# Optimization experiments

Measured on AMD Instinct MI355X. Metric: run time of the kernel, lower is better.

Reference implementation:

```python
import jax, jax.numpy as jnp
import numpy as np
import math

IN_CH = 32
OUT_CH = 32
NODE_NUM = 24
BATCH = 32768
# skeleton edges: self-loops + chain (parent -> child), matching init_kwargs
_SRC = list(range(24)) + list(range(23))
_DST = list(range(24)) + list(range(1, 24))


def _build_mask():
    # block mask: block (dst, src) of size [OUT_CH, IN_CH] set to 1 per edge
    m = np.zeros((OUT_CH * NODE_NUM, IN_CH * NODE_NUM), dtype=np.float32)
    for s, d in zip(_SRC, _DST):
        m[OUT_CH * d:OUT_CH * (d + 1), IN_CH * s:IN_CH * (s + 1)] = 1.0
    return jnp.asarray(m)


def setup_inputs() -> dict:
    key = jax.random.key(0)
    kx, kw, kb = jax.random.split(key, 3)
    mask = _build_mask()
    dim = IN_CH * NODE_NUM
    # kaiming-uniform-like per-block init approximated by scaled normal; only
    # values inside mask blocks matter (forward multiplies by mask anyway)
    weight = jax.random.normal(kw, (OUT_CH * NODE_NUM, dim), dtype=jnp.float32) * (1.0 / math.sqrt(IN_CH))
    bound = 1.0 / math.sqrt(dim)
    bias = jax.random.uniform(kb, (OUT_CH * NODE_NUM,), dtype=jnp.float32, minval=-bound, maxval=bound)
    x = jax.random.normal(kx, (BATCH, dim), dtype=jnp.float32)
    return {"x": x, "weight": weight, "bias": bias, "mask": mask}


def reference(x, weight, bias, mask):
    # F.linear(x, weight * mask, bias) == x @ (weight*mask)^T + bias
    w = weight * mask
    return jnp.einsum("bi,oi->bo", x, w) + bias
```

## Files before the change

kernel.cpp:

```cpp
#include <hip/hip_runtime.h>
#include <hip/hip_bf16.h>


typedef __bf16 bf16x8 __attribute__((ext_vector_type(8)));
typedef float  f32x4  __attribute__((ext_vector_type(4)));

#define DIM 768
#define STRIDE 772
#define NFRAG (24 * 2 * 2)

__device__ __forceinline__ bf16x8 cvt8(const float* __restrict__ p) {
    float4 lo = *(const float4*)p;
    float4 hi = *(const float4*)(p + 4);
    bf16x8 r;
    r[0] = (__bf16)lo.x; r[1] = (__bf16)lo.y; r[2] = (__bf16)lo.z; r[3] = (__bf16)lo.w;
    r[4] = (__bf16)hi.x; r[5] = (__bf16)hi.y; r[6] = (__bf16)hi.z; r[7] = (__bf16)hi.w;
    return r;
}

__device__ __forceinline__ bf16x8 cvt8r(float4 lo, float4 hi) {
    bf16x8 r;
    r[0] = (__bf16)lo.x; r[1] = (__bf16)lo.y; r[2] = (__bf16)lo.z; r[3] = (__bf16)lo.w;
    r[4] = (__bf16)hi.x; r[5] = (__bf16)hi.y; r[6] = (__bf16)hi.z; r[7] = (__bf16)hi.w;
    return r;
}

__global__ void prepack_w_kernel(const float* __restrict__ w, bf16x8* __restrict__ ws)
{
    const int fid = blockIdx.x * 256 + threadIdx.x;
    const int lane = fid & 63;
    const int ni   = (fid >> 6) & 1;
    const int kt   = (fid >> 7) & 1;
    const int d    = fid >> 8;
    const int quad = lane >> 4, l16 = lane & 15;

    bf16x8 v;
    if (d == 0 && kt == 0) {
#pragma unroll
        for (int j = 0; j < 8; ++j) v[j] = (__bf16)0.f;
    } else {
        const float* src = w + (long)(32 * d + 16 * ni + l16) * DIM
                             + (32 * d - 32 + 32 * kt + 8 * quad);
        v = cvt8(src);
    }
    ws[fid] = v;
}

__global__ __launch_bounds__(512, 4)
void skeleton_linear_kernel(const float* __restrict__ x,
                            const float* __restrict__ bias,
                            const bf16x8* __restrict__ wfrag,
                            float* __restrict__ out)
{
    __shared__ float lds[16 * STRIDE];

    const int tid  = threadIdx.x;
    const int lane = tid & 63;
    const int wave = tid >> 6;
    const int quad = lane >> 4;
    const int l16  = lane & 15;
    const long row = (long)blockIdx.x * 16 + l16;

    const float* xr = x + row * DIM + 8 * quad;
    float4 lo[4], hi[4];
#pragma unroll
    for (int s = 0; s < 4; ++s) {
        int kb = 32 * (3 * wave - 1 + s);
        if (kb < 0) kb = 0;
        lo[s] = *(const float4*)(xr + kb);
        hi[s] = *(const float4*)(xr + kb + 4);
    }

    bf16x8 xf[4];
#pragma unroll
    for (int s = 0; s < 4; ++s) xf[s] = cvt8r(lo[s], hi[s]);

#pragma unroll
    for (int i = 0; i < 3; ++i) {
        const int d = 3 * wave + i;
        f32x4 acc0 = *(const f32x4*)(bias + 32 * d + 4 * quad);
        f32x4 acc1 = *(const f32x4*)(bias + 32 * d + 16 + 4 * quad);
#pragma unroll
        for (int kt = 0; kt < 2; ++kt) {
            const int fb = (d * 2 + kt) * 2 * 64 + lane;
            acc0 = __builtin_amdgcn_mfma_f32_16x16x32_bf16(wfrag[fb],      xf[i + kt], acc0, 0, 0, 0);
            acc1 = __builtin_amdgcn_mfma_f32_16x16x32_bf16(wfrag[fb + 64], xf[i + kt], acc1, 0, 0, 0);
        }
        *(f32x4*)&lds[l16 * STRIDE + 32 * d + 4 * quad]      = acc0;
        *(f32x4*)&lds[l16 * STRIDE + 32 * d + 16 + 4 * quad] = acc1;
    }
    __syncthreads();

    {
        float* go = out + (long)blockIdx.x * 16 * DIM;
#pragma unroll
        for (int i = 0; i < 6; ++i) {
            int f = tid + 512 * i;
            int r = f / 192, c4 = f % 192;
            float4 v = *(const float4*)&lds[r * STRIDE + 4 * c4];
            *(float4*)(go + (long)r * DIM + 4 * c4) = v;
        }
    }
}

extern "C" void kernel_launch(void* const* d_in, const int* in_sizes, int n_in,
                              void* d_out, int out_size, void* d_ws, size_t ws_size,
                              hipStream_t stream) {
    const float* x    = (const float*)d_in[0];
    const float* w    = (const float*)d_in[1];
    const float* bias = (const float*)d_in[2];
    float* out = (float*)d_out;

    bf16x8* wpack = (bf16x8*)d_ws;

    prepack_w_kernel<<<NFRAG * 64 / 256, 256, 0, stream>>>(w, wpack);

    const int BATCH = 32768;
    dim3 grid(BATCH / 16);
    skeleton_linear_kernel<<<grid, 512, 0, stream>>>(x, bias, wpack, out);
}
```

Measured before the change: 190.1 us.

## Process two row strips per block with prefetch of next strip's inputs

Each block now handles two 16-row strips in sequence, loading the second strip's x values from global memory while the first strip is converted, multiplied and stored. This halves the grid size and aims to overlap global load latency with MFMA compute and output stores. It also raises the launch-bounds occupancy hint from 4 to 6 blocks, which puts pressure on registers. The cost is an extra barrier between strips and more live registers per thread.

```diff
diff --git a/kernel.cpp b/kernel.cpp
--- a/kernel.cpp
+++ b/kernel.cpp
@@ -8,6 +8,7 @@
 #define DIM 768
 #define STRIDE 772
 #define NFRAG (24 * 2 * 2)
+#define SPB 2
 
 __device__ __forceinline__ bf16x8 cvt8(const float* __restrict__ p) {
     float4 lo = *(const float4*)p;
@@ -46,7 +47,7 @@
     ws[fid] = v;
 }
 
-__global__ __launch_bounds__(512, 4)
+__global__ __launch_bounds__(512, 6)
 void skeleton_linear_kernel(const float* __restrict__ x,
                             const float* __restrict__ bias,
                             const bf16x8* __restrict__ wfrag,
@@ -59,47 +60,66 @@
     const int wave = tid >> 6;
     const int quad = lane >> 4;
     const int l16  = lane & 15;
-    const long row = (long)blockIdx.x * 16 + l16;
+    const long row0 = (long)blockIdx.x * (16 * SPB) + l16;
 
-    const float* xr = x + row * DIM + 8 * quad;
+    int kb[4];
+#pragma unroll
+    for (int s = 0; s < 4; ++s) {
+        int k = 32 * (3 * wave - 1 + s);
+        kb[s] = k < 0 ? 0 : k;
+    }
+
+    const float* xr = x + row0 * DIM + 8 * quad;
+
     float4 lo[4], hi[4];
 #pragma unroll
     for (int s = 0; s < 4; ++s) {
-        int kb = 32 * (3 * wave - 1 + s);
-        if (kb < 0) kb = 0;
-        lo[s] = *(const float4*)(xr + kb);
-        hi[s] = *(const float4*)(xr + kb + 4);
+        lo[s] = *(const float4*)(xr + kb[s]);
+        hi[s] = *(const float4*)(xr + kb[s] + 4);
     }
 
-    bf16x8 xf[4];
 #pragma unroll
-    for (int s = 0; s < 4; ++s) xf[s] = cvt8r(lo[s], hi[s]);
+    for (int t = 0; t < SPB; ++t) {
+        bf16x8 xf[4];
+#pragma unroll
+        for (int s = 0; s < 4; ++s) xf[s] = cvt8r(lo[s], hi[s]);
+
+        if (t + 1 < SPB) {
+            const float* xn = xr + (long)(t + 1) * 16 * DIM;
+#pragma unroll
+            for (int s = 0; s < 4; ++s) {
+                lo[s] = *(const float4*)(xn + kb[s]);
+                hi[s] = *(const float4*)(xn + kb[s] + 4);
+            }
+        }
 
 #pragma unroll
-    for (int i = 0; i < 3; ++i) {
-        const int d = 3 * wave + i;
-        f32x4 acc0 = *(const f32x4*)(bias + 32 * d + 4 * quad);
-        f32x4 acc1 = *(const f32x4*)(bias + 32 * d + 16 + 4 * quad);
+        for (int i = 0; i < 3; ++i) {
+            const int d = 3 * wave + i;
+            f32x4 acc0 = *(const f32x4*)(bias + 32 * d + 4 * quad);
+            f32x4 acc1 = *(const f32x4*)(bias + 32 * d + 16 + 4 * quad);
 #pragma unroll
-        for (int kt = 0; kt < 2; ++kt) {
-            const int fb = (d * 2 + kt) * 2 * 64 + lane;
-            acc0 = __builtin_amdgcn_mfma_f32_16x16x32_bf16(wfrag[fb],      xf[i + kt], acc0, 0, 0, 0);
-            acc1 = __builtin_amdgcn_mfma_f32_16x16x32_bf16(wfrag[fb + 64], xf[i + kt], acc1, 0, 0, 0);
+            for (int kt = 0; kt < 2; ++kt) {
+                const int fb = (d * 2 + kt) * 2 * 64 + lane;
+                acc0 = __builtin_amdgcn_mfma_f32_16x16x32_bf16(wfrag[fb],      xf[i + kt], acc0, 0, 0, 0);
+                acc1 = __builtin_amdgcn_mfma_f32_16x16x32_bf16(wfrag[fb + 64], xf[i + kt], acc1, 0, 0, 0);
+            }
+            *(f32x4*)&lds[l16 * STRIDE + 32 * d + 4 * quad]      = acc0;
+            *(f32x4*)&lds[l16 * STRIDE + 32 * d + 16 + 4 * quad] = acc1;
         }
-        *(f32x4*)&lds[l16 * STRIDE + 32 * d + 4 * quad]      = acc0;
-        *(f32x4*)&lds[l16 * STRIDE + 32 * d + 16 + 4 * quad] = acc1;
-    }
-    __syncthreads();
+        __syncthreads();
 
-    {
-        float* go = out + (long)blockIdx.x * 16 * DIM;
+        {
+            float* go = out + ((long)blockIdx.x * (16 * SPB) + 16 * t) * DIM;
 #pragma unroll
-        for (int i = 0; i < 6; ++i) {
-            int f = tid + 512 * i;
-            int r = f / 192, c4 = f % 192;
-            float4 v = *(const float4*)&lds[r * STRIDE + 4 * c4];
-            *(float4*)(go + (long)r * DIM + 4 * c4) = v;
+            for (int i2 = 0; i2 < 6; ++i2) {
+                int f = tid + 512 * i2;
+                int r = f / 192, c4 = f % 192;
+                float4 v = *(const float4*)&lds[r * STRIDE + 4 * c4];
+                *(float4*)(go + (long)r * DIM + 4 * c4) = v;
+            }
         }
+        if (t + 1 < SPB) __syncthreads();
     }
 }
 
@@ -116,6 +136,6 @@
     prepack_w_kernel<<<NFRAG * 64 / 256, 256, 0, stream>>>(w, wpack);
 
     const int BATCH = 32768;
-    dim3 grid(BATCH / 16);
+    dim3 grid(BATCH / (16 * SPB));
     skeleton_linear_kernel<<<grid, 512, 0, stream>>>(x, bias, wpack, out);
 }
```

Result: slower. 201.1 us (+5.8%).
